# Optimization experiments

Hardware: AMD Instinct MI355X
Metric: run time of the kernel (lower is better)

## Reference

```python
import jax, jax.numpy as jnp
import numpy as np

B, S, E = 1, 8192, 1024

def setup_inputs() -> dict:
    key = jax.random.key(0)
    ks = jax.random.split(key, 7)
    scale = 1.0 / np.sqrt(E)
    q = jax.random.normal(ks[0], (B, S, E), dtype=jnp.float32)
    Wq = jax.random.uniform(ks[1], (E, E), jnp.float32, -scale, scale)
    bq = jax.random.uniform(ks[2], (E,), jnp.float32, -scale, scale)
    Wk = jax.random.uniform(ks[3], (E, E), jnp.float32, -scale, scale)
    bk = jax.random.uniform(ks[4], (E,), jnp.float32, -scale, scale)
    Wv = jax.random.uniform(ks[5], (E, E), jnp.float32, -scale, scale)
    bv = jax.random.uniform(ks[6], (E,), jnp.float32, -scale, scale)
    return {"q": q, "Wq": Wq, "bq": bq, "Wk": Wk, "bk": bk, "Wv": Wv, "bv": bv}

def reference(q, Wq, bq, Wk, bk, Wv, bv):
    # k and v default to q in the original module
    Q = jnp.einsum('bse,fe->bsf', q, Wq) + bq          # [B,S,E]
    K = jnp.einsum('bse,fe->bsf', q, Wk) + bk          # [B,S,E]
    V = jnp.einsum('bse,fe->bsf', q, Wv) + bv          # [B,S,E]
    weights = jax.nn.softmax(K, axis=1)                # softmax over sequence dim
    # sum over seq -> [B,E], then sum over E keepdim -> [B,1] (faithful to source)
    weighted_context = jnp.sum(weights * V, axis=1).sum(axis=1, keepdims=True)
    Y = jax.nn.sigmoid(Q) * weighted_context           # broadcast (valid since B==1)
    return Y
```

## Files before the change

kernel.cpp:

```cpp
#include <hip/hip_runtime.h>
#include <hip/hip_bf16.h>
#include <stdint.h>

typedef __bf16 bf16_t;
typedef __bf16 bf16x8 __attribute__((ext_vector_type(8)));
typedef float f32x4 __attribute__((ext_vector_type(4)));

#define NKT 16

__device__ __forceinline__ void gload_lds16(const void* g, void* l) {
  using gptr_t = const __attribute__((address_space(1))) void*;
  using lptr_t = __attribute__((address_space(3))) void*;
  gptr_t gp = (gptr_t)(uintptr_t)g;
  lptr_t lp = (lptr_t)(uint32_t)(uintptr_t)l;
  __builtin_amdgcn_global_load_lds(gp, lp, 16, 0, 0);
}

__device__ __forceinline__ bf16x8 cvt8v(const float* __restrict__ src, int i8) {
  const float4* s = reinterpret_cast<const float4*>(src) + (size_t)i8 * 2;
  float4 a = s[0], b = s[1];
  bf16x8 o;
  o[0] = (bf16_t)a.x; o[1] = (bf16_t)a.y; o[2] = (bf16_t)a.z; o[3] = (bf16_t)a.w;
  o[4] = (bf16_t)b.x; o[5] = (bf16_t)b.y; o[6] = (bf16_t)b.z; o[7] = (bf16_t)b.w;
  return o;
}

__global__ __launch_bounds__(256) void cvt_all(const float* __restrict__ q,
                                               const float* __restrict__ Wk,
                                               const float* __restrict__ Wv,
                                               const float* __restrict__ Wq,
                                               const float* __restrict__ bk,
                                               const float* __restrict__ bv,
                                               bf16_t* __restrict__ qb,
                                               bf16_t* __restrict__ Wkv,
                                               bf16_t* __restrict__ Wqb,
                                               float* __restrict__ bkv) {
  const int b = blockIdx.x;
  const int t = threadIdx.x;
  if (b < 4096) {
    int i = b * 256 + t;
    *reinterpret_cast<bf16x8*>(qb + (size_t)i * 8) = cvt8v(q, i);
  } else if (b < 4608) {
    int i = (b - 4096) * 256 + t;
    int j = i >> 7, c8 = i & 127;
    *reinterpret_cast<bf16x8*>(Wkv + (size_t)j * 2048 + c8 * 8) = cvt8v(Wk, i);
  } else if (b < 5120) {
    int i = (b - 4608) * 256 + t;
    int j = i >> 7, c8 = i & 127;
    *reinterpret_cast<bf16x8*>(Wkv + (size_t)j * 2048 + 1024 + c8 * 8) = cvt8v(Wv, i);
  } else if (b < 5632) {
    int i = (b - 5120) * 256 + t;
    *reinterpret_cast<bf16x8*>(Wqb + (size_t)i * 8) = cvt8v(Wq, i);
  } else {
#pragma unroll
    for (int u = 0; u < 4; ++u) {
      int j = t * 4 + u;
      bkv[2 * j] = bk[j];
      bkv[2 * j + 1] = bv[j];
    }
  }
}

__global__ __launch_bounds__(512, 1) void gemm_kv8(const bf16_t* __restrict__ A,
                                                   const bf16_t* __restrict__ Bkv,
                                                   const float* __restrict__ bkv,
                                                   float* __restrict__ pden,
                                                   float* __restrict__ pnum) {
  __shared__ bf16_t lA[2 * 256 * 64];
  __shared__ bf16_t lB[2 * 256 * 64];
  __shared__ float sD[2][128];
  __shared__ float sN[2][128];

  const int tid = threadIdx.x;
  const int w = tid >> 6, l = tid & 63;
  const int wr = w >> 2, wc = w & 3;
  const int swz = (blockIdx.x & 7) * 32 + (blockIdx.x >> 3);
  const int bx = swz & 7, by = swz >> 3;
  const int m0 = by * 256, n0 = bx * 256;

  const int rl3 = l >> 3;
  const int scol = ((l & 7) ^ rl3) * 8;
  const int fr = l & 15, fg = l >> 4, sw = l & 7;

  const bf16_t* Ab = A + (size_t)(m0 + w * 8 + rl3) * 1024 + scol;
  const bf16_t* Bb = Bkv + (size_t)(n0 + w * 8 + rl3) * 1024 + scol;

  f32x4 acc[8][4];
#pragma unroll
  for (int m = 0; m < 8; ++m)
#pragma unroll
    for (int n = 0; n < 4; ++n) acc[m][n] = (f32x4){0.f, 0.f, 0.f, 0.f};

#define STAGE_A(kt, h, r, slot)                                              \
  gload_lds16(Ab + (size_t)((h) * 128 + (r) * 64) * 1024 + (kt) * 64,        \
              &lA[(slot) * 16384 + ((h) * 128 + (r) * 64 + w * 8) * 64])
#define STAGE_B(kt, h, r, slot)                                              \
  gload_lds16(Bb + (size_t)((h) * 128 + (r) * 64) * 1024 + (kt) * 64,        \
              &lB[(slot) * 16384 + ((h) * 128 + (r) * 64 + w * 8) * 64])
#define RD_A(mm, ks) \
  (*reinterpret_cast<const bf16x8*>(&lA[aBase + ((mm) * 16 + fr) * 64 + ((((ks) * 4) + fg) ^ sw) * 8]))
#define RD_B(nn, ks) \
  (*reinterpret_cast<const bf16x8*>(&lB[bBase + ((nn) * 16 + fr) * 64 + ((((ks) * 4) + fg) ^ sw) * 8]))

  STAGE_A(0, 0, 0, 0); STAGE_A(0, 0, 1, 0); STAGE_A(0, 1, 0, 0); STAGE_A(0, 1, 1, 0);
  STAGE_B(0, 0, 0, 0); STAGE_B(0, 0, 1, 0); STAGE_B(0, 1, 0, 0); STAGE_B(0, 1, 1, 0);

#pragma unroll 1
  for (int T = 0; T < NKT; ++T) {
    const int slot = T & 1, ns = slot ^ 1;
    const bool pf = (T + 1) < NKT;
    if (pf) { STAGE_A(T + 1, 0, 0, ns); STAGE_A(T + 1, 0, 1, ns); }
    if (pf) asm volatile("s_waitcnt vmcnt(2)" ::: "memory");
    else    asm volatile("s_waitcnt vmcnt(0)" ::: "memory");
    __builtin_amdgcn_s_barrier();
    __builtin_amdgcn_sched_barrier(0);

    const int aBase = slot * 16384 + wr * 8192;
    const int bBase = slot * 16384 + wc * 4096;
    bf16x8 af[4], bfv[4];
#pragma unroll
    for (int n = 0; n < 4; ++n) bfv[n] = RD_B(n, 0);
#pragma unroll
    for (int m = 0; m < 4; ++m) af[m] = RD_A(m, 0);
    if (pf) { STAGE_A(T + 1, 1, 0, ns); STAGE_A(T + 1, 1, 1, ns); }
    __builtin_amdgcn_s_setprio(1);
#pragma unroll
    for (int m = 0; m < 4; ++m)
#pragma unroll
      for (int n = 0; n < 4; ++n)
        acc[m][n] = __builtin_amdgcn_mfma_f32_16x16x32_bf16(af[m], bfv[n], acc[m][n], 0, 0, 0);
    __builtin_amdgcn_s_setprio(0);
    __builtin_amdgcn_s_barrier();
    __builtin_amdgcn_sched_barrier(0);
#pragma unroll
    for (int m = 0; m < 4; ++m) af[m] = RD_A(m + 4, 0);
    if (pf) { STAGE_B(T + 1, 0, 0, ns); STAGE_B(T + 1, 0, 1, ns); }
    __builtin_amdgcn_s_setprio(1);
#pragma unroll
    for (int m = 0; m < 4; ++m)
#pragma unroll
      for (int n = 0; n < 4; ++n)
        acc[m + 4][n] = __builtin_amdgcn_mfma_f32_16x16x32_bf16(af[m], bfv[n], acc[m + 4][n], 0, 0, 0);
    __builtin_amdgcn_s_setprio(0);
    __builtin_amdgcn_s_barrier();
    __builtin_amdgcn_sched_barrier(0);
#pragma unroll
    for (int n = 0; n < 4; ++n) bfv[n] = RD_B(n, 1);
#pragma unroll
    for (int m = 0; m < 4; ++m) af[m] = RD_A(m, 1);
    if (pf) { STAGE_B(T + 1, 1, 0, ns); STAGE_B(T + 1, 1, 1, ns); }
    __builtin_amdgcn_s_setprio(1);
#pragma unroll
    for (int m = 0; m < 4; ++m)
#pragma unroll
      for (int n = 0; n < 4; ++n)
        acc[m][n] = __builtin_amdgcn_mfma_f32_16x16x32_bf16(af[m], bfv[n], acc[m][n], 0, 0, 0);
    __builtin_amdgcn_s_setprio(0);
    __builtin_amdgcn_s_barrier();
    __builtin_amdgcn_sched_barrier(0);
#pragma unroll
    for (int m = 0; m < 4; ++m) af[m] = RD_A(m + 4, 1);
    __builtin_amdgcn_s_setprio(1);
#pragma unroll
    for (int m = 0; m < 4; ++m)
#pragma unroll
      for (int n = 0; n < 4; ++n)
        acc[m + 4][n] = __builtin_amdgcn_mfma_f32_16x16x32_bf16(af[m], bfv[n], acc[m + 4][n], 0, 0, 0);
    __builtin_amdgcn_s_setprio(0);
    __builtin_amdgcn_s_barrier();
    __builtin_amdgcn_sched_barrier(0);
  }
#undef STAGE_A
#undef STAGE_B
#undef RD_A
#undef RD_B

  float dpn[4] = {0.f, 0.f, 0.f, 0.f};
  float npn[4] = {0.f, 0.f, 0.f, 0.f};
#pragma unroll
  for (int n = 0; n < 4; ++n) {
    const int col = n0 + wc * 64 + n * 16 + fr;
    const float bc = bkv[col];
#pragma unroll
    for (int m = 0; m < 8; ++m)
#pragma unroll
      for (int r = 0; r < 4; ++r) {
        float x = acc[m][n][r] + bc;
        float xp = __shfl_xor(x, 1);
        float e = __expf(x);
        dpn[n] += e;
        npn[n] += e * xp;
      }
    dpn[n] += __shfl_xor(dpn[n], 16); dpn[n] += __shfl_xor(dpn[n], 32);
    npn[n] += __shfl_xor(npn[n], 16); npn[n] += __shfl_xor(npn[n], 32);
  }
  if (l < 16 && (l & 1) == 0) {
#pragma unroll
    for (int n = 0; n < 4; ++n) {
      sD[wr][wc * 32 + n * 8 + (l >> 1)] = dpn[n];
      sN[wr][wc * 32 + n * 8 + (l >> 1)] = npn[n];
    }
  }
  __syncthreads();
  if (tid < 128) {
    pden[(size_t)by * 1024 + bx * 128 + tid] = sD[0][tid] + sD[1][tid];
    pnum[(size_t)by * 1024 + bx * 128 + tid] = sN[0][tid] + sN[1][tid];
  }
}

__global__ __launch_bounds__(512, 1) void gemm_q8(const bf16_t* __restrict__ A,
                                                  const bf16_t* __restrict__ Bq,
                                                  const float* __restrict__ bias,
                                                  const float* __restrict__ pden,
                                                  const float* __restrict__ pnum,
                                                  float* __restrict__ C) {
  __shared__ bf16_t lA[2 * 256 * 64];
  __shared__ bf16_t lB[2 * 128 * 64];
  __shared__ float red[512];

  const int tid = threadIdx.x;
  const int w = tid >> 6, l = tid & 63;
  const int wr = w >> 1, wc = w & 1;
  const int swz = (blockIdx.x & 7) * 32 + (blockIdx.x >> 3);
  const int bx = swz & 7, by = swz >> 3;
  const int m0 = by * 256, n0 = bx * 128;

  const int rl3 = l >> 3;
  const int scol = ((l & 7) ^ rl3) * 8;
  const int fr = l & 15, fg = l >> 4, sw = l & 7;

  const bf16_t* Ab = A + (size_t)(m0 + w * 8 + rl3) * 1024 + scol;
  const bf16_t* Bb = Bq + (size_t)(n0 + w * 8 + rl3) * 1024 + scol;

  f32x4 acc[4][4];
#pragma unroll
  for (int m = 0; m < 4; ++m)
#pragma unroll
    for (int n = 0; n < 4; ++n) acc[m][n] = (f32x4){0.f, 0.f, 0.f, 0.f};

#define STAGE_A(kt, h, r, slot)                                              \
  gload_lds16(Ab + (size_t)((h) * 128 + (r) * 64) * 1024 + (kt) * 64,        \
              &lA[(slot) * 16384 + ((h) * 128 + (r) * 64 + w * 8) * 64])
#define STAGE_B(kt, h, slot)                                                 \
  gload_lds16(Bb + (size_t)((h) * 64) * 1024 + (kt) * 64,                    \
              &lB[(slot) * 8192 + ((h) * 64 + w * 8) * 64])
#define RD_A(mm, ks) \
  (*reinterpret_cast<const bf16x8*>(&lA[aBase + ((mm) * 16 + fr) * 64 + ((((ks) * 4) + fg) ^ sw) * 8]))
#define RD_B(nn, ks) \
  (*reinterpret_cast<const bf16x8*>(&lB[bBase + ((nn) * 16 + fr) * 64 + ((((ks) * 4) + fg) ^ sw) * 8]))

  STAGE_A(0, 0, 0, 0); STAGE_A(0, 0, 1, 0); STAGE_A(0, 1, 0, 0); STAGE_A(0, 1, 1, 0);
  STAGE_B(0, 0, 0); STAGE_B(0, 1, 0);

  float vsum = 0.f;
#pragma unroll
  for (int j = 0; j < 2; ++j) {
    const int c = tid + j * 512;
    float d = 0.f, nm = 0.f;
#pragma unroll 8
    for (int b2 = 0; b2 < 32; ++b2) {
      d += pden[b2 * 1024 + c];
      nm += pnum[b2 * 1024 + c];
    }
    vsum += nm / d;
  }
  red[tid] = vsum;
  __syncthreads();
  for (int s = 256; s > 0; s >>= 1) {
    if (tid < s) red[tid] += red[tid + s];
    __syncthreads();
  }
  const float cv = red[0];

#pragma unroll 1
  for (int T = 0; T < NKT; ++T) {
    const int slot = T & 1, ns = slot ^ 1;
    const bool pf = (T + 1) < NKT;
    if (pf) { STAGE_A(T + 1, 0, 0, ns); STAGE_A(T + 1, 0, 1, ns); }
    if (pf) asm volatile("s_waitcnt vmcnt(2)" ::: "memory");
    else    asm volatile("s_waitcnt vmcnt(0)" ::: "memory");
    __builtin_amdgcn_s_barrier();
    __builtin_amdgcn_sched_barrier(0);

    const int aBase = slot * 16384 + wr * 4096;
    const int bBase = slot * 8192 + wc * 4096;
    bf16x8 af[2], bfv[4];
#pragma unroll
    for (int n = 0; n < 4; ++n) bfv[n] = RD_B(n, 0);
    af[0] = RD_A(0, 0); af[1] = RD_A(1, 0);
    if (pf) { STAGE_A(T + 1, 1, 0, ns); STAGE_A(T + 1, 1, 1, ns); }
    __builtin_amdgcn_s_setprio(1);
#pragma unroll
    for (int m = 0; m < 2; ++m)
#pragma unroll
      for (int n = 0; n < 4; ++n)
        acc[m][n] = __builtin_amdgcn_mfma_f32_16x16x32_bf16(af[m], bfv[n], acc[m][n], 0, 0, 0);
    __builtin_amdgcn_s_setprio(0);
    __builtin_amdgcn_s_barrier();
    __builtin_amdgcn_sched_barrier(0);
    af[0] = RD_A(2, 0); af[1] = RD_A(3, 0);
    if (pf) STAGE_B(T + 1, 0, ns);
    __builtin_amdgcn_s_setprio(1);
#pragma unroll
    for (int m = 0; m < 2; ++m)
#pragma unroll
      for (int n = 0; n < 4; ++n)
        acc[m + 2][n] = __builtin_amdgcn_mfma_f32_16x16x32_bf16(af[m], bfv[n], acc[m + 2][n], 0, 0, 0);
    __builtin_amdgcn_s_setprio(0);
    __builtin_amdgcn_s_barrier();
    __builtin_amdgcn_sched_barrier(0);
#pragma unroll
    for (int n = 0; n < 4; ++n) bfv[n] = RD_B(n, 1);
    af[0] = RD_A(0, 1); af[1] = RD_A(1, 1);
    if (pf) STAGE_B(T + 1, 1, ns);
    __builtin_amdgcn_s_setprio(1);
#pragma unroll
    for (int m = 0; m < 2; ++m)
#pragma unroll
      for (int n = 0; n < 4; ++n)
        acc[m][n] = __builtin_amdgcn_mfma_f32_16x16x32_bf16(af[m], bfv[n], acc[m][n], 0, 0, 0);
    __builtin_amdgcn_s_setprio(0);
    __builtin_amdgcn_s_barrier();
    __builtin_amdgcn_sched_barrier(0);
    af[0] = RD_A(2, 1); af[1] = RD_A(3, 1);
    __builtin_amdgcn_s_setprio(1);
#pragma unroll
    for (int m = 0; m < 2; ++m)
#pragma unroll
      for (int n = 0; n < 4; ++n)
        acc[m + 2][n] = __builtin_amdgcn_mfma_f32_16x16x32_bf16(af[m], bfv[n], acc[m + 2][n], 0, 0, 0);
    __builtin_amdgcn_s_setprio(0);
    __builtin_amdgcn_s_barrier();
    __builtin_amdgcn_sched_barrier(0);
  }
#undef STAGE_A
#undef STAGE_B
#undef RD_A
#undef RD_B

#pragma unroll
  for (int n = 0; n < 4; ++n) {
    const int col = n0 + wc * 64 + n * 16 + fr;
    const float bs = bias[col];
#pragma unroll
    for (int m = 0; m < 4; ++m) {
      const int row = m0 + wr * 64 + m * 16 + fg * 4;
#pragma unroll
      for (int r = 0; r < 4; ++r) {
        float v = acc[m][n][r] + bs;
        v = cv / (1.f + __expf(-v));
        C[(size_t)(row + r) * 1024 + col] = v;
      }
    }
  }
}

extern "C" void kernel_launch(void* const* d_in, const int* in_sizes, int n_in,
                              void* d_out, int out_size, void* d_ws, size_t ws_size,
                              hipStream_t stream) {
  const float* q = (const float*)d_in[0];
  const float* Wq = (const float*)d_in[1];
  const float* bq = (const float*)d_in[2];
  const float* Wk = (const float*)d_in[3];
  const float* bk = (const float*)d_in[4];
  const float* Wv = (const float*)d_in[5];
  const float* bv = (const float*)d_in[6];
  float* out = (float*)d_out;

  char* ws = (char*)d_ws;
  bf16_t* qb = (bf16_t*)ws;
  bf16_t* Wkv = (bf16_t*)(ws + (size_t)16 * 1024 * 1024);
  bf16_t* Wqb = (bf16_t*)(ws + (size_t)20 * 1024 * 1024);
  float* bkv = (float*)(ws + (size_t)22 * 1024 * 1024);
  float* pden = (float*)(ws + (size_t)23 * 1024 * 1024);
  float* pnum = (float*)(ws + (size_t)23 * 1024 * 1024 + 131072);

  cvt_all<<<5633, 256, 0, stream>>>(q, Wk, Wv, Wq, bk, bv, qb, Wkv, Wqb, bkv);
  gemm_kv8<<<256, 512, 0, stream>>>(qb, Wkv, bkv, pden, pnum);
  gemm_q8<<<256, 512, 0, stream>>>(qb, Wqb, bq, pden, pnum, out);
}
```

Before: 77.44 us.

## Switch both GEMMs to 32x32x16 bf16 MFMA with halved barrier phases

Both the K/V and Q GEMM kernels move from 16x16x32 MFMA tiles to 32x32x16 tiles. Fragment loads, the LDS read indexing and the epilogue row/column mapping are rewritten to match the 32x32 accumulator layout. Each K-tile now has two compute phases instead of four, so there are fewer barriers, and the global-to-LDS prefetch issue is regrouped. Larger MFMA tiles cut LDS read traffic per FLOP and the instruction count, but the longer phases between barriers give less room to overlap the prefetch.

```diff
diff --git a/kernel.cpp b/kernel.cpp
--- a/kernel.cpp
+++ b/kernel.cpp
@@ -4,7 +4,7 @@
 
 typedef __bf16 bf16_t;
 typedef __bf16 bf16x8 __attribute__((ext_vector_type(8)));
-typedef float f32x4 __attribute__((ext_vector_type(4)));
+typedef float f32x16 __attribute__((ext_vector_type(16)));
 
 #define NKT 16
 
@@ -61,11 +61,11 @@
   }
 }
 
-__global__ __launch_bounds__(512, 1) void gemm_kv8(const bf16_t* __restrict__ A,
-                                                   const bf16_t* __restrict__ Bkv,
-                                                   const float* __restrict__ bkv,
-                                                   float* __restrict__ pden,
-                                                   float* __restrict__ pnum) {
+__global__ __launch_bounds__(512, 1) void gemm_kv32(const bf16_t* __restrict__ A,
+                                                    const bf16_t* __restrict__ Bkv,
+                                                    const float* __restrict__ bkv,
+                                                    float* __restrict__ pden,
+                                                    float* __restrict__ pnum) {
   __shared__ bf16_t lA[2 * 256 * 64];
   __shared__ bf16_t lB[2 * 256 * 64];
   __shared__ float sD[2][128];
@@ -73,23 +73,23 @@
 
   const int tid = threadIdx.x;
   const int w = tid >> 6, l = tid & 63;
-  const int wr = w >> 2, wc = w & 3;
+  const int kwr = w >> 2, kwc = w & 3;
   const int swz = (blockIdx.x & 7) * 32 + (blockIdx.x >> 3);
   const int bx = swz & 7, by = swz >> 3;
   const int m0 = by * 256, n0 = bx * 256;
 
   const int rl3 = l >> 3;
   const int scol = ((l & 7) ^ rl3) * 8;
-  const int fr = l & 15, fg = l >> 4, sw = l & 7;
+  const int l31 = l & 31, lhi = l >> 5, sw = l & 7;
 
   const bf16_t* Ab = A + (size_t)(m0 + w * 8 + rl3) * 1024 + scol;
   const bf16_t* Bb = Bkv + (size_t)(n0 + w * 8 + rl3) * 1024 + scol;
 
-  f32x4 acc[8][4];
-#pragma unroll
-  for (int m = 0; m < 8; ++m)
-#pragma unroll
-    for (int n = 0; n < 4; ++n) acc[m][n] = (f32x4){0.f, 0.f, 0.f, 0.f};
+  f32x16 acc[4][2];
+#pragma unroll
+  for (int m = 0; m < 4; ++m)
+#pragma unroll
+    for (int n = 0; n < 2; ++n) acc[m][n] = (f32x16){0.f};
 
 #define STAGE_A(kt, h, r, slot)                                              \
   gload_lds16(Ab + (size_t)((h) * 128 + (r) * 64) * 1024 + (kt) * 64,        \
@@ -97,10 +97,10 @@
 #define STAGE_B(kt, h, r, slot)                                              \
   gload_lds16(Bb + (size_t)((h) * 128 + (r) * 64) * 1024 + (kt) * 64,        \
               &lB[(slot) * 16384 + ((h) * 128 + (r) * 64 + w * 8) * 64])
-#define RD_A(mm, ks) \
-  (*reinterpret_cast<const bf16x8*>(&lA[aBase + ((mm) * 16 + fr) * 64 + ((((ks) * 4) + fg) ^ sw) * 8]))
-#define RD_B(nn, ks) \
-  (*reinterpret_cast<const bf16x8*>(&lB[bBase + ((nn) * 16 + fr) * 64 + ((((ks) * 4) + fg) ^ sw) * 8]))
+#define RD_A(mt, ks) \
+  (*reinterpret_cast<const bf16x8*>(&lA[slot * 16384 + (kwr * 128 + (mt) * 32 + l31) * 64 + ((((ks) * 2) + lhi) ^ sw) * 8]))
+#define RD_B(nt, ks) \
+  (*reinterpret_cast<const bf16x8*>(&lB[slot * 16384 + (kwc * 64 + (nt) * 32 + l31) * 64 + ((((ks) * 2) + lhi) ^ sw) * 8]))
 
   STAGE_A(0, 0, 0, 0); STAGE_A(0, 0, 1, 0); STAGE_A(0, 1, 0, 0); STAGE_A(0, 1, 1, 0);
   STAGE_B(0, 0, 0, 0); STAGE_B(0, 0, 1, 0); STAGE_B(0, 1, 0, 0); STAGE_B(0, 1, 1, 0);
@@ -115,57 +115,37 @@
     __builtin_amdgcn_s_barrier();
     __builtin_amdgcn_sched_barrier(0);
 
-    const int aBase = slot * 16384 + wr * 8192;
-    const int bBase = slot * 16384 + wc * 4096;
-    bf16x8 af[4], bfv[4];
-#pragma unroll
-    for (int n = 0; n < 4; ++n) bfv[n] = RD_B(n, 0);
-#pragma unroll
-    for (int m = 0; m < 4; ++m) af[m] = RD_A(m, 0);
-    if (pf) { STAGE_A(T + 1, 1, 0, ns); STAGE_A(T + 1, 1, 1, ns); }
+    bf16x8 af[4], ag[4], b0[2], b1[2];
+#pragma unroll
+    for (int nt = 0; nt < 2; ++nt) { b0[nt] = RD_B(nt, 0); b1[nt] = RD_B(nt, 1); }
+#pragma unroll
+    for (int mt = 0; mt < 4; ++mt) { af[mt] = RD_A(mt, 0); ag[mt] = RD_A(mt, 1); }
+    if (pf) { STAGE_A(T + 1, 1, 0, ns); STAGE_A(T + 1, 1, 1, ns);
+              STAGE_B(T + 1, 0, 0, ns); STAGE_B(T + 1, 0, 1, ns); }
     __builtin_amdgcn_s_setprio(1);
 #pragma unroll
-    for (int m = 0; m < 4; ++m)
-#pragma unroll
-      for (int n = 0; n < 4; ++n)
-        acc[m][n] = __builtin_amdgcn_mfma_f32_16x16x32_bf16(af[m], bfv[n], acc[m][n], 0, 0, 0);
+    for (int mt = 0; mt < 4; ++mt)
+#pragma unroll
+      for (int nt = 0; nt < 2; ++nt) {
+        acc[mt][nt] = __builtin_amdgcn_mfma_f32_32x32x16_bf16(af[mt], b0[nt], acc[mt][nt], 0, 0, 0);
+        acc[mt][nt] = __builtin_amdgcn_mfma_f32_32x32x16_bf16(ag[mt], b1[nt], acc[mt][nt], 0, 0, 0);
+      }
     __builtin_amdgcn_s_setprio(0);
     __builtin_amdgcn_s_barrier();
     __builtin_amdgcn_sched_barrier(0);
 #pragma unroll
-    for (int m = 0; m < 4; ++m) af[m] = RD_A(m + 4, 0);
-    if (pf) { STAGE_B(T + 1, 0, 0, ns); STAGE_B(T + 1, 0, 1, ns); }
-    __builtin_amdgcn_s_setprio(1);
-#pragma unroll
-    for (int m = 0; m < 4; ++m)
-#pragma unroll
-      for (int n = 0; n < 4; ++n)
-        acc[m + 4][n] = __builtin_amdgcn_mfma_f32_16x16x32_bf16(af[m], bfv[n], acc[m + 4][n], 0, 0, 0);
-    __builtin_amdgcn_s_setprio(0);
-    __builtin_amdgcn_s_barrier();
-    __builtin_amdgcn_sched_barrier(0);
-#pragma unroll
-    for (int n = 0; n < 4; ++n) bfv[n] = RD_B(n, 1);
-#pragma unroll
-    for (int m = 0; m < 4; ++m) af[m] = RD_A(m, 1);
+    for (int nt = 0; nt < 2; ++nt) { b0[nt] = RD_B(nt, 2); b1[nt] = RD_B(nt, 3); }
+#pragma unroll
+    for (int mt = 0; mt < 4; ++mt) { af[mt] = RD_A(mt, 2); ag[mt] = RD_A(mt, 3); }
     if (pf) { STAGE_B(T + 1, 1, 0, ns); STAGE_B(T + 1, 1, 1, ns); }
     __builtin_amdgcn_s_setprio(1);
 #pragma unroll
-    for (int m = 0; m < 4; ++m)
-#pragma unroll
-      for (int n = 0; n < 4; ++n)
-        acc[m][n] = __builtin_amdgcn_mfma_f32_16x16x32_bf16(af[m], bfv[n], acc[m][n], 0, 0, 0);
-    __builtin_amdgcn_s_setprio(0);
-    __builtin_amdgcn_s_barrier();
-    __builtin_amdgcn_sched_barrier(0);
-#pragma unroll
-    for (int m = 0; m < 4; ++m) af[m] = RD_A(m + 4, 1);
-    __builtin_amdgcn_s_setprio(1);
-#pragma unroll
-    for (int m = 0; m < 4; ++m)
-#pragma unroll
-      for (int n = 0; n < 4; ++n)
-        acc[m + 4][n] = __builtin_amdgcn_mfma_f32_16x16x32_bf16(af[m], bfv[n], acc[m + 4][n], 0, 0, 0);
+    for (int mt = 0; mt < 4; ++mt)
+#pragma unroll
+      for (int nt = 0; nt < 2; ++nt) {
+        acc[mt][nt] = __builtin_amdgcn_mfma_f32_32x32x16_bf16(af[mt], b0[nt], acc[mt][nt], 0, 0, 0);
+        acc[mt][nt] = __builtin_amdgcn_mfma_f32_32x32x16_bf16(ag[mt], b1[nt], acc[mt][nt], 0, 0, 0);
+      }
     __builtin_amdgcn_s_setprio(0);
     __builtin_amdgcn_s_barrier();
     __builtin_amdgcn_sched_barrier(0);
@@ -175,30 +155,30 @@
 #undef RD_A
 #undef RD_B
 
-  float dpn[4] = {0.f, 0.f, 0.f, 0.f};
-  float npn[4] = {0.f, 0.f, 0.f, 0.f};
-#pragma unroll
-  for (int n = 0; n < 4; ++n) {
-    const int col = n0 + wc * 64 + n * 16 + fr;
+  float dpn[2] = {0.f, 0.f};
+  float npn[2] = {0.f, 0.f};
+#pragma unroll
+  for (int nt = 0; nt < 2; ++nt) {
+    const int col = n0 + kwc * 64 + nt * 32 + l31;
     const float bc = bkv[col];
 #pragma unroll
-    for (int m = 0; m < 8; ++m)
-#pragma unroll
-      for (int r = 0; r < 4; ++r) {
-        float x = acc[m][n][r] + bc;
+    for (int mt = 0; mt < 4; ++mt)
+#pragma unroll
+      for (int r = 0; r < 16; ++r) {
+        float x = acc[mt][nt][r] + bc;
         float xp = __shfl_xor(x, 1);
         float e = __expf(x);
-        dpn[n] += e;
-        npn[n] += e * xp;
-      }
-    dpn[n] += __shfl_xor(dpn[n], 16); dpn[n] += __shfl_xor(dpn[n], 32);
-    npn[n] += __shfl_xor(npn[n], 16); npn[n] += __shfl_xor(npn[n], 32);
-  }
-  if (l < 16 && (l & 1) == 0) {
-#pragma unroll
-    for (int n = 0; n < 4; ++n) {
-      sD[wr][wc * 32 + n * 8 + (l >> 1)] = dpn[n];
-      sN[wr][wc * 32 + n * 8 + (l >> 1)] = npn[n];
+        dpn[nt] += e;
+        npn[nt] += e * xp;
+      }
+    dpn[nt] += __shfl_xor(dpn[nt], 32);
+    npn[nt] += __shfl_xor(npn[nt], 32);
+  }
+  if (l < 32 && (l & 1) == 0) {
+#pragma unroll
+    for (int nt = 0; nt < 2; ++nt) {
+      sD[kwr][kwc * 32 + nt * 16 + (l >> 1)] = dpn[nt];
+      sN[kwr][kwc * 32 + nt * 16 + (l >> 1)] = npn[nt];
     }
   }
   __syncthreads();
@@ -208,35 +188,35 @@
   }
 }
 
-__global__ __launch_bounds__(512, 1) void gemm_q8(const bf16_t* __restrict__ A,
-                                                  const bf16_t* __restrict__ Bq,
-                                                  const float* __restrict__ bias,
-                                                  const float* __restrict__ pden,
-                                                  const float* __restrict__ pnum,
-                                                  float* __restrict__ C) {
+__global__ __launch_bounds__(512, 1) void gemm_q32(const bf16_t* __restrict__ A,
+                                                   const bf16_t* __restrict__ Bq,
+                                                   const float* __restrict__ bias,
+                                                   const float* __restrict__ pden,
+                                                   const float* __restrict__ pnum,
+                                                   float* __restrict__ C) {
   __shared__ bf16_t lA[2 * 256 * 64];
   __shared__ bf16_t lB[2 * 128 * 64];
   __shared__ float red[512];
 
   const int tid = threadIdx.x;
   const int w = tid >> 6, l = tid & 63;
-  const int wr = w >> 1, wc = w & 1;
+  const int qwr = w >> 1, qwc = w & 1;
   const int swz = (blockIdx.x & 7) * 32 + (blockIdx.x >> 3);
   const int bx = swz & 7, by = swz >> 3;
   const int m0 = by * 256, n0 = bx * 128;
 
   const int rl3 = l >> 3;
   const int scol = ((l & 7) ^ rl3) * 8;
-  const int fr = l & 15, fg = l >> 4, sw = l & 7;
+  const int l31 = l & 31, lhi = l >> 5, sw = l & 7;
 
   const bf16_t* Ab = A + (size_t)(m0 + w * 8 + rl3) * 1024 + scol;
   const bf16_t* Bb = Bq + (size_t)(n0 + w * 8 + rl3) * 1024 + scol;
 
-  f32x4 acc[4][4];
-#pragma unroll
-  for (int m = 0; m < 4; ++m)
-#pragma unroll
-    for (int n = 0; n < 4; ++n) acc[m][n] = (f32x4){0.f, 0.f, 0.f, 0.f};
+  f32x16 acc[2][2];
+#pragma unroll
+  for (int m = 0; m < 2; ++m)
+#pragma unroll
+    for (int n = 0; n < 2; ++n) acc[m][n] = (f32x16){0.f};
 
 #define STAGE_A(kt, h, r, slot)                                              \
   gload_lds16(Ab + (size_t)((h) * 128 + (r) * 64) * 1024 + (kt) * 64,        \
@@ -244,10 +224,10 @@
 #define STAGE_B(kt, h, slot)                                                 \
   gload_lds16(Bb + (size_t)((h) * 64) * 1024 + (kt) * 64,                    \
               &lB[(slot) * 8192 + ((h) * 64 + w * 8) * 64])
-#define RD_A(mm, ks) \
-  (*reinterpret_cast<const bf16x8*>(&lA[aBase + ((mm) * 16 + fr) * 64 + ((((ks) * 4) + fg) ^ sw) * 8]))
-#define RD_B(nn, ks) \
-  (*reinterpret_cast<const bf16x8*>(&lB[bBase + ((nn) * 16 + fr) * 64 + ((((ks) * 4) + fg) ^ sw) * 8]))
+#define RD_A(mt, ks) \
+  (*reinterpret_cast<const bf16x8*>(&lA[slot * 16384 + (qwr * 64 + (mt) * 32 + l31) * 64 + ((((ks) * 2) + lhi) ^ sw) * 8]))
+#define RD_B(nt, ks) \
+  (*reinterpret_cast<const bf16x8*>(&lB[slot * 8192 + (qwc * 64 + (nt) * 32 + l31) * 64 + ((((ks) * 2) + lhi) ^ sw) * 8]))
 
   STAGE_A(0, 0, 0, 0); STAGE_A(0, 0, 1, 0); STAGE_A(0, 1, 0, 0); STAGE_A(0, 1, 1, 0);
   STAGE_B(0, 0, 0); STAGE_B(0, 1, 0);
@@ -282,53 +262,36 @@
     __builtin_amdgcn_s_barrier();
     __builtin_amdgcn_sched_barrier(0);
 
-    const int aBase = slot * 16384 + wr * 4096;
-    const int bBase = slot * 8192 + wc * 4096;
-    bf16x8 af[2], bfv[4];
-#pragma unroll
-    for (int n = 0; n < 4; ++n) bfv[n] = RD_B(n, 0);
-    af[0] = RD_A(0, 0); af[1] = RD_A(1, 0);
-    if (pf) { STAGE_A(T + 1, 1, 0, ns); STAGE_A(T + 1, 1, 1, ns); }
+    bf16x8 af[2], ag[2], b0[2], b1[2];
+#pragma unroll
+    for (int nt = 0; nt < 2; ++nt) { b0[nt] = RD_B(nt, 0); b1[nt] = RD_B(nt, 1); }
+#pragma unroll
+    for (int mt = 0; mt < 2; ++mt) { af[mt] = RD_A(mt, 0); ag[mt] = RD_A(mt, 1); }
+    if (pf) { STAGE_A(T + 1, 1, 0, ns); STAGE_A(T + 1, 1, 1, ns); STAGE_B(T + 1, 0, ns); }
     __builtin_amdgcn_s_setprio(1);
 #pragma unroll
-    for (int m = 0; m < 2; ++m)
-#pragma unroll
-      for (int n = 0; n < 4; ++n)
-        acc[m][n] = __builtin_amdgcn_mfma_f32_16x16x32_bf16(af[m], bfv[n], acc[m][n], 0, 0, 0);
+    for (int mt = 0; mt < 2; ++mt)
+#pragma unroll
+      for (int nt = 0; nt < 2; ++nt) {
+        acc[mt][nt] = __builtin_amdgcn_mfma_f32_32x32x16_bf16(af[mt], b0[nt], acc[mt][nt], 0, 0, 0);
+        acc[mt][nt] = __builtin_amdgcn_mfma_f32_32x32x16_bf16(ag[mt], b1[nt], acc[mt][nt], 0, 0, 0);
+      }
     __builtin_amdgcn_s_setprio(0);
     __builtin_amdgcn_s_barrier();
     __builtin_amdgcn_sched_barrier(0);
-    af[0] = RD_A(2, 0); af[1] = RD_A(3, 0);
-    if (pf) STAGE_B(T + 1, 0, ns);
-    __builtin_amdgcn_s_setprio(1);
-#pragma unroll
-    for (int m = 0; m < 2; ++m)
-#pragma unroll
-      for (int n = 0; n < 4; ++n)
-        acc[m + 2][n] = __builtin_amdgcn_mfma_f32_16x16x32_bf16(af[m], bfv[n], acc[m + 2][n], 0, 0, 0);
-    __builtin_amdgcn_s_setprio(0);
-    __builtin_amdgcn_s_barrier();
-    __builtin_amdgcn_sched_barrier(0);
-#pragma unroll
-    for (int n = 0; n < 4; ++n) bfv[n] = RD_B(n, 1);
-    af[0] = RD_A(0, 1); af[1] = RD_A(1, 1);
+#pragma unroll
+    for (int nt = 0; nt < 2; ++nt) { b0[nt] = RD_B(nt, 2); b1[nt] = RD_B(nt, 3); }
+#pragma unroll
+    for (int mt = 0; mt < 2; ++mt) { af[mt] = RD_A(mt, 2); ag[mt] = RD_A(mt, 3); }
     if (pf) STAGE_B(T + 1, 1, ns);
     __builtin_amdgcn_s_setprio(1);
 #pragma unroll
-    for (int m = 0; m < 2; ++m)
-#pragma unroll
-      for (int n = 0; n < 4; ++n)
-        acc[m][n] = __builtin_amdgcn_mfma_f32_16x16x32_bf16(af[m], bfv[n], acc[m][n], 0, 0, 0);
-    __builtin_amdgcn_s_setprio(0);
-    __builtin_amdgcn_s_barrier();
-    __builtin_amdgcn_sched_barrier(0);
-    af[0] = RD_A(2, 1); af[1] = RD_A(3, 1);
-    __builtin_amdgcn_s_setprio(1);
-#pragma unroll
-    for (int m = 0; m < 2; ++m)
-#pragma unroll
-      for (int n = 0; n < 4; ++n)
-        acc[m + 2][n] = __builtin_amdgcn_mfma_f32_16x16x32_bf16(af[m], bfv[n], acc[m + 2][n], 0, 0, 0);
+    for (int mt = 0; mt < 2; ++mt)
+#pragma unroll
+      for (int nt = 0; nt < 2; ++nt) {
+        acc[mt][nt] = __builtin_amdgcn_mfma_f32_32x32x16_bf16(af[mt], b0[nt], acc[mt][nt], 0, 0, 0);
+        acc[mt][nt] = __builtin_amdgcn_mfma_f32_32x32x16_bf16(ag[mt], b1[nt], acc[mt][nt], 0, 0, 0);
+      }
     __builtin_amdgcn_s_setprio(0);
     __builtin_amdgcn_s_barrier();
     __builtin_amdgcn_sched_barrier(0);
@@ -339,17 +302,18 @@
 #undef RD_B
 
 #pragma unroll
-  for (int n = 0; n < 4; ++n) {
-    const int col = n0 + wc * 64 + n * 16 + fr;
+  for (int nt = 0; nt < 2; ++nt) {
+    const int col = n0 + qwc * 64 + nt * 32 + l31;
     const float bs = bias[col];
 #pragma unroll
-    for (int m = 0; m < 4; ++m) {
-      const int row = m0 + wr * 64 + m * 16 + fg * 4;
-#pragma unroll
-      for (int r = 0; r < 4; ++r) {
-        float v = acc[m][n][r] + bs;
+    for (int mt = 0; mt < 2; ++mt) {
+      const int rbase = m0 + qwr * 64 + mt * 32 + 4 * lhi;
+#pragma unroll
+      for (int r = 0; r < 16; ++r) {
+        const int row = rbase + (r & 3) + 8 * (r >> 2);
+        float v = acc[mt][nt][r] + bs;
         v = cv / (1.f + __expf(-v));
-        C[(size_t)(row + r) * 1024 + col] = v;
+        C[(size_t)row * 1024 + col] = v;
       }
     }
   }
@@ -376,6 +340,6 @@
   float* pnum = (float*)(ws + (size_t)23 * 1024 * 1024 + 131072);
 
   cvt_all<<<5633, 256, 0, stream>>>(q, Wk, Wv, Wq, bk, bv, qb, Wkv, Wqb, bkv);
-  gemm_kv8<<<256, 512, 0, stream>>>(qb, Wkv, bkv, pden, pnum);
-  gemm_q8<<<256, 512, 0, stream>>>(qb, Wqb, bq, pden, pnum, out);
-}
+  gemm_kv32<<<256, 512, 0, stream>>>(qb, Wkv, bkv, pden, pnum);
+  gemm_q32<<<256, 512, 0, stream>>>(qb, Wqb, bq, pden, pnum, out);
+}
```

After: 83.56 us. +7.9%, slower.
